# Performance work log

Measured on AMD Instinct MI355X. Metric: run time of the kernel, lower is better.

Reference implementation:

```python
import jax, jax.numpy as jnp
import numpy as np

B, I, H = 512, 256, 512
UNFOLDS = 6


def setup_inputs() -> dict:
    key = jax.random.key(0)
    ks = jax.random.split(key, 13)
    u = lambda k, shape, lo, hi: jax.random.uniform(k, shape, jnp.float32, lo, hi)
    sensory_erev = (2.0 * jax.random.randint(ks[3], (I, H), 0, 2) - 1.0).astype(jnp.float32)
    erev = (2.0 * jax.random.randint(ks[7], (H, H), 0, 2) - 1.0).astype(jnp.float32)
    return {
        "inputs": jax.random.normal(ks[0], (B, I), jnp.float32),
        "state": jax.random.normal(ks[1], (B, H), jnp.float32),
        "sensory_mu": u(ks[2], (I, H), 0.3, 0.8),
        "sensory_sigma": u(ks[4], (I, H), 3.0, 8.0),
        "sensory_W": u(ks[5], (I, H), 0.01, 1.0),
        "sensory_erev": sensory_erev,
        "mu": u(ks[6], (H, H), 0.3, 0.8),
        "sigma": u(ks[8], (H, H), 3.0, 8.0),
        "W": u(ks[9], (H, H), 0.01, 1.0),
        "erev": erev,
        "vleak": u(ks[10], (H,), -0.2, 0.2),
        "gleak": jnp.ones((H,), jnp.float32),
        "cm": jnp.full((H,), 0.5, jnp.float32),
    }


def reference(inputs, state, sensory_mu, sensory_sigma, sensory_W, sensory_erev,
              mu, sigma, W, erev, vleak, gleak, cm):
    # Sensory synapse currents (computed once): (B, I, H) broadcast
    sensory_act = jax.nn.sigmoid((inputs[:, :, None] - sensory_mu[None]) * sensory_sigma[None])
    sensory_w_act = sensory_W[None] * sensory_act                      # (B, I, H)
    w_num_sensory = jnp.sum(sensory_w_act * sensory_erev[None], axis=1)  # (B, H)
    w_den_sensory = jnp.sum(sensory_w_act, axis=1)                        # (B, H)

    def step(v_pre, _):
        # recurrent synapse gating: (B, H_pre, H_post)
        act = jax.nn.sigmoid((v_pre[:, :, None] - mu[None]) * sigma[None])
        w_act = W[None] * act
        w_num = jnp.sum(w_act * erev[None], axis=1) + w_num_sensory
        w_den = jnp.sum(w_act, axis=1) + w_den_sensory
        numerator = cm * v_pre + gleak * vleak + w_num
        denominator = cm + gleak + w_den
        return numerator / (denominator + 1e-8), None

    v_pre, _ = jax.lax.scan(step, state, None, length=UNFOLDS)
    return v_pre
```

## Files before the change

kernel.cpp:

```cpp
#include <hip/hip_runtime.h>

#define LTC_B 512
#define LTC_H 512
#define LTC_I 256

static constexpr float kL2E = 1.4426950408889634f;

struct alignas(8)  H4   { _Float16 a, c, wz, wd; };
struct alignas(16) H4x2 { H4 e[2]; };

typedef unsigned int u32;
#define AS_G __attribute__((address_space(1)))
#define AS_L __attribute__((address_space(3)))

__device__ __forceinline__ void ldg_lds16(const void* g, void* l) {
    __builtin_amdgcn_global_load_lds((const AS_G u32*)g, (AS_L u32*)l, 16, 0, 0);
}

__global__ void ltc_prep(const float* __restrict__ mu, const float* __restrict__ sigma,
                         const float* __restrict__ W, const float* __restrict__ erev,
                         H4x2* __restrict__ slab, int K) {
    int idx = blockIdx.x * 256 + threadIdx.x;
    if (idx >= K * LTC_H) return;
    int j = idx >> 9, h = idx & 511;
    float sg = sigma[idx], m = mu[idx], w = W[idx], ev = erev[idx];
    H4 o;
    o.a  = (_Float16)(-sg * kL2E);
    o.c  = (_Float16)(m * sg * kL2E);
    o.wz = (_Float16)(w * ev);
    o.wd = (_Float16)(w);
    slab[((h >> 6) * (K >> 1) + (j >> 1)) * 64 + (h & 63)].e[j & 1] = o;
}

template<int K, bool RECUR>
__global__ __launch_bounds__(256, 4)
void ltc_pass(const float* __restrict__ vsrc,
              const H4x2* __restrict__ slab,
              const float* __restrict__ snum, const float* __restrict__ sden,
              const float* __restrict__ vleak, const float* __restrict__ gleak,
              const float* __restrict__ cm,
              float* __restrict__ onum, float* __restrict__ oden,
              float* __restrict__ vout)
{
    __shared__ H4x2 wbuf[2][16 * 64];
    const int tid  = threadIdx.x;
    const int lane = tid & 63;
    const int wave = tid >> 6;
    const int ht   = blockIdx.x;
    const int b    = blockIdx.y * 4 + wave;

    constexpr int NG = K / 64;
    float vr[NG];
    #pragma unroll
    for (int g = 0; g < NG; ++g) vr[g] = vsrc[b * K + g * 64 + lane];

    const char* slabt = (const char*)slab + (size_t)ht * (K * 512);
    constexpr int NC = K / 32;
    float n = 0.f, d = 0.f;

    {
        char* dst = (char*)&wbuf[0][0];
        #pragma unroll
        for (int r = 0; r < 4; ++r) {
            const int row = wave * 4 + r;
            ldg_lds16(slabt + row * 1024 + lane * 16, dst + row * 1024);
        }
    }

    #pragma unroll
    for (int c = 0; c < NC; ++c) {
        __syncthreads();
        if (c + 1 < NC) {
            const char* src = slabt + (c + 1) * 16384;
            char* dst = (char*)&wbuf[(c + 1) & 1][0];
            #pragma unroll
            for (int r = 0; r < 4; ++r) {
                const int row = wave * 4 + r;
                ldg_lds16(src + row * 1024 + lane * 16, dst + row * 1024);
            }
        }
        const H4x2* wb = &wbuf[c & 1][0];
        constexpr int dummy = 0; (void)dummy;
        const int g = c >> 1;
        const int joff = (c & 1) * 32;
        #pragma unroll
        for (int jj = 0; jj < 16; ++jj) {
            H4x2 pr = wb[jj * 64 + lane];
            float vj0 = __int_as_float(__builtin_amdgcn_readlane(__float_as_int(vr[g]), joff + jj * 2));
            float vj1 = __int_as_float(__builtin_amdgcn_readlane(__float_as_int(vr[g]), joff + jj * 2 + 1));
            float t0 = fmaf((float)pr.e[0].a, vj0, (float)pr.e[0].c);
            float t1 = fmaf((float)pr.e[1].a, vj1, (float)pr.e[1].c);
            float e0 = __builtin_amdgcn_exp2f(t0);
            float e1 = __builtin_amdgcn_exp2f(t1);
            float s0 = __builtin_amdgcn_rcpf(1.0f + e0);
            float s1 = __builtin_amdgcn_rcpf(1.0f + e1);
            n = fmaf((float)pr.e[0].wz, s0, n);
            d = fmaf((float)pr.e[0].wd, s0, d);
            n = fmaf((float)pr.e[1].wz, s1, n);
            d = fmaf((float)pr.e[1].wd, s1, d);
        }
    }

    const int h  = ht * 64 + lane;
    const int bh = b * LTC_H + h;
    if constexpr (RECUR) {
        const float gl = gleak[h], vl = vleak[h], c0 = cm[h];
        const float vp = vsrc[bh];
        float num = fmaf(c0, vp, gl * vl) + n + snum[bh];
        float den = c0 + gl + d + sden[bh];
        vout[bh] = num * __builtin_amdgcn_rcpf(den + 1e-8f);
    } else {
        onum[bh] = n;
        oden[bh] = d;
    }
}

extern "C" void kernel_launch(void* const* d_in, const int* in_sizes, int n_in,
                              void* d_out, int out_size, void* d_ws, size_t ws_size,
                              hipStream_t stream) {
    const float* inputs = (const float*)d_in[0];
    const float* state  = (const float*)d_in[1];
    const float* smu    = (const float*)d_in[2];
    const float* ssig   = (const float*)d_in[3];
    const float* sW     = (const float*)d_in[4];
    const float* serev  = (const float*)d_in[5];
    const float* mu     = (const float*)d_in[6];
    const float* sig    = (const float*)d_in[7];
    const float* W      = (const float*)d_in[8];
    const float* erev   = (const float*)d_in[9];
    const float* vleak  = (const float*)d_in[10];
    const float* gleak  = (const float*)d_in[11];
    const float* cm     = (const float*)d_in[12];

    float* out  = (float*)d_out;
    char*  ws   = (char*)d_ws;
    float* snum = (float*)(ws);
    float* sden = (float*)(ws + 1 * 1048576);
    float* vA   = (float*)(ws + 2 * 1048576);
    H4x2*  rslab = (H4x2*)(ws + 3 * 1048576);
    H4x2*  sslab = (H4x2*)(ws + 5 * 1048576);

    ltc_prep<<<(LTC_H * LTC_H + 255) / 256, 256, 0, stream>>>(mu, sig, W, erev, rslab, LTC_H);
    ltc_prep<<<(LTC_I * LTC_H + 255) / 256, 256, 0, stream>>>(smu, ssig, sW, serev, sslab, LTC_I);

    dim3 grid(LTC_H / 64, LTC_B / 4);
    dim3 blk(256);

    ltc_pass<LTC_I, false><<<grid, blk, 0, stream>>>(
        inputs, sslab, nullptr, nullptr, nullptr, nullptr, nullptr,
        snum, sden, nullptr);

    const float* vin = state;
    float* targets[6] = {vA, out, vA, out, vA, out};
    for (int s = 0; s < 6; ++s) {
        ltc_pass<LTC_H, true><<<grid, blk, 0, stream>>>(
            vin, rslab, snum, sden, vleak, gleak, cm,
            nullptr, nullptr, targets[s]);
        vin = targets[s];
    }
}
```

Before: 336.1 us.

## Repack slab as paired halves, rotate chunk order, share one reciprocal per pair

Repacks the fp16 parameter slab so each 16-byte element holds the a/c/wz/wd values for two j rows, and the prep kernel writes it coalesced with one thread per pair. The pass kernel starts its chunk loop at a rotation that depends on the block index, to spread concurrent blocks across different slab regions. It reads the pre-activations as wave-uniform scalar loads from memory instead of readlane from registers, preloads all 16 pairs from LDS before computing, and replaces two reciprocals with one reciprocal of the product plus two multiplies. The aim is fewer transcendental ops and less L2 hotspotting, at the cost of more registers and a slightly different rounding.

```diff
diff --git a/kernel.cpp b/kernel.cpp
--- a/kernel.cpp
+++ b/kernel.cpp
@@ -6,8 +6,7 @@
 
 static constexpr float kL2E = 1.4426950408889634f;
 
-struct alignas(8)  H4   { _Float16 a, c, wz, wd; };
-struct alignas(16) H4x2 { H4 e[2]; };
+struct alignas(16) HPair { _Float16 a0, a1, c0, c1, wz0, wz1, wd0, wd1; };
 
 typedef unsigned int u32;
 #define AS_G __attribute__((address_space(1)))
@@ -17,87 +16,99 @@
     __builtin_amdgcn_global_load_lds((const AS_G u32*)g, (AS_L u32*)l, 16, 0, 0);
 }
 
+template<int K>
 __global__ void ltc_prep(const float* __restrict__ mu, const float* __restrict__ sigma,
                          const float* __restrict__ W, const float* __restrict__ erev,
-                         H4x2* __restrict__ slab, int K) {
-    int idx = blockIdx.x * 256 + threadIdx.x;
-    if (idx >= K * LTC_H) return;
-    int j = idx >> 9, h = idx & 511;
-    float sg = sigma[idx], m = mu[idx], w = W[idx], ev = erev[idx];
-    H4 o;
-    o.a  = (_Float16)(-sg * kL2E);
-    o.c  = (_Float16)(m * sg * kL2E);
-    o.wz = (_Float16)(w * ev);
-    o.wd = (_Float16)(w);
-    slab[((h >> 6) * (K >> 1) + (j >> 1)) * 64 + (h & 63)].e[j & 1] = o;
+                         HPair* __restrict__ slab) {
+    const int t = blockIdx.x * 256 + threadIdx.x;
+    if (t >= K * 256) return;
+    const int hh   = t & 63;
+    const int rest = t >> 6;
+    const int jp   = rest & (K / 2 - 1);
+    const int ht   = rest / (K / 2);
+    const int h    = ht * 64 + hh;
+    const int g0   = (2 * jp) * LTC_H + h;
+    const int g1   = g0 + LTC_H;
+    HPair o;
+    o.a0 = (_Float16)(-sigma[g0] * kL2E);
+    o.a1 = (_Float16)(-sigma[g1] * kL2E);
+    o.c0 = (_Float16)(mu[g0] * sigma[g0] * kL2E);
+    o.c1 = (_Float16)(mu[g1] * sigma[g1] * kL2E);
+    o.wz0 = (_Float16)(W[g0] * erev[g0]);
+    o.wz1 = (_Float16)(W[g1] * erev[g1]);
+    o.wd0 = (_Float16)(W[g0]);
+    o.wd1 = (_Float16)(W[g1]);
+    slab[t] = o;
 }
 
 template<int K, bool RECUR>
 __global__ __launch_bounds__(256, 4)
 void ltc_pass(const float* __restrict__ vsrc,
-              const H4x2* __restrict__ slab,
+              const HPair* __restrict__ slab,
               const float* __restrict__ snum, const float* __restrict__ sden,
               const float* __restrict__ vleak, const float* __restrict__ gleak,
               const float* __restrict__ cm,
               float* __restrict__ onum, float* __restrict__ oden,
               float* __restrict__ vout)
 {
-    __shared__ H4x2 wbuf[2][16 * 64];
+    __shared__ HPair wbuf[2][16 * 64];
     const int tid  = threadIdx.x;
     const int lane = tid & 63;
-    const int wave = tid >> 6;
+    const int wu   = __builtin_amdgcn_readfirstlane(tid >> 6);
     const int ht   = blockIdx.x;
-    const int b    = blockIdx.y * 4 + wave;
+    const int b    = blockIdx.y * 4 + wu;
+    const float* __restrict__ vrow = vsrc + (size_t)b * K;
 
-    constexpr int NG = K / 64;
-    float vr[NG];
-    #pragma unroll
-    for (int g = 0; g < NG; ++g) vr[g] = vsrc[b * K + g * 64 + lane];
-
+    constexpr int NC = K / 32;
+    const int rot = (int)((blockIdx.x + 7u * blockIdx.y) & (NC - 1));
     const char* slabt = (const char*)slab + (size_t)ht * (K * 512);
-    constexpr int NC = K / 32;
-    float n = 0.f, d = 0.f;
 
     {
-        char* dst = (char*)&wbuf[0][0];
+        const char* src = slabt + rot * 16384 + wu * 4096;
+        char* dst = (char*)&wbuf[0][0] + wu * 4096;
         #pragma unroll
-        for (int r = 0; r < 4; ++r) {
-            const int row = wave * 4 + r;
-            ldg_lds16(slabt + row * 1024 + lane * 16, dst + row * 1024);
-        }
+        for (int rr = 0; rr < 4; ++rr)
+            ldg_lds16(src + rr * 1024 + lane * 16, dst + rr * 1024);
     }
 
+    float na = 0.f, da = 0.f;
+
     #pragma unroll
-    for (int c = 0; c < NC; ++c) {
+    for (int i = 0; i < NC; ++i) {
+        const int c = (rot + i) & (NC - 1);
         __syncthreads();
-        if (c + 1 < NC) {
-            const char* src = slabt + (c + 1) * 16384;
-            char* dst = (char*)&wbuf[(c + 1) & 1][0];
+        if (i + 1 < NC) {
+            const int cn = (rot + i + 1) & (NC - 1);
+            const char* src = slabt + cn * 16384 + wu * 4096;
+            char* dst = (char*)&wbuf[(i + 1) & 1][0] + wu * 4096;
             #pragma unroll
-            for (int r = 0; r < 4; ++r) {
-                const int row = wave * 4 + r;
-                ldg_lds16(src + row * 1024 + lane * 16, dst + row * 1024);
-            }
+            for (int rr = 0; rr < 4; ++rr)
+                ldg_lds16(src + rr * 1024 + lane * 16, dst + rr * 1024);
         }
-        const H4x2* wb = &wbuf[c & 1][0];
-        constexpr int dummy = 0; (void)dummy;
-        const int g = c >> 1;
-        const int joff = (c & 1) * 32;
+        const HPair* wb = &wbuf[i & 1][0];
+        const float* __restrict__ vch = vrow + c * 32;
+
+        HPair pr[16];
+        #pragma unroll
+        for (int jj = 0; jj < 16; ++jj) pr[jj] = wb[jj * 64 + lane];
+
         #pragma unroll
         for (int jj = 0; jj < 16; ++jj) {
-            H4x2 pr = wb[jj * 64 + lane];
-            float vj0 = __int_as_float(__builtin_amdgcn_readlane(__float_as_int(vr[g]), joff + jj * 2));
-            float vj1 = __int_as_float(__builtin_amdgcn_readlane(__float_as_int(vr[g]), joff + jj * 2 + 1));
-            float t0 = fmaf((float)pr.e[0].a, vj0, (float)pr.e[0].c);
-            float t1 = fmaf((float)pr.e[1].a, vj1, (float)pr.e[1].c);
-            float e0 = __builtin_amdgcn_exp2f(t0);
-            float e1 = __builtin_amdgcn_exp2f(t1);
-            float s0 = __builtin_amdgcn_rcpf(1.0f + e0);
-            float s1 = __builtin_amdgcn_rcpf(1.0f + e1);
-            n = fmaf((float)pr.e[0].wz, s0, n);
-            d = fmaf((float)pr.e[0].wd, s0, d);
-            n = fmaf((float)pr.e[1].wz, s1, n);
-            d = fmaf((float)pr.e[1].wd, s1, d);
+            const float vj0 = vch[2 * jj];
+            const float vj1 = vch[2 * jj + 1];
+            const float t0 = fmaf((float)pr[jj].a0, vj0, (float)pr[jj].c0);
+            const float t1 = fmaf((float)pr[jj].a1, vj1, (float)pr[jj].c1);
+            const float e0 = __builtin_amdgcn_exp2f(t0);
+            const float e1 = __builtin_amdgcn_exp2f(t1);
+            const float d0 = 1.0f + e0;
+            const float d1 = 1.0f + e1;
+            const float rr = __builtin_amdgcn_rcpf(d0 * d1);
+            const float s0 = rr * d1;
+            const float s1 = rr * d0;
+            na = fmaf((float)pr[jj].wz0, s0, na);
+            da = fmaf((float)pr[jj].wd0, s0, da);
+            na = fmaf((float)pr[jj].wz1, s1, na);
+            da = fmaf((float)pr[jj].wd1, s1, da);
         }
     }
 
@@ -106,12 +117,12 @@
     if constexpr (RECUR) {
         const float gl = gleak[h], vl = vleak[h], c0 = cm[h];
         const float vp = vsrc[bh];
-        float num = fmaf(c0, vp, gl * vl) + n + snum[bh];
-        float den = c0 + gl + d + sden[bh];
+        const float num = fmaf(c0, vp, gl * vl) + na + snum[bh];
+        const float den = c0 + gl + da + sden[bh];
         vout[bh] = num * __builtin_amdgcn_rcpf(den + 1e-8f);
     } else {
-        onum[bh] = n;
-        oden[bh] = d;
+        onum[bh] = na;
+        oden[bh] = da;
     }
 }
 
@@ -137,11 +148,11 @@
     float* snum = (float*)(ws);
     float* sden = (float*)(ws + 1 * 1048576);
     float* vA   = (float*)(ws + 2 * 1048576);
-    H4x2*  rslab = (H4x2*)(ws + 3 * 1048576);
-    H4x2*  sslab = (H4x2*)(ws + 5 * 1048576);
+    HPair* rslab = (HPair*)(ws + 3 * 1048576);
+    HPair* sslab = (HPair*)(ws + 5 * 1048576);
 
-    ltc_prep<<<(LTC_H * LTC_H + 255) / 256, 256, 0, stream>>>(mu, sig, W, erev, rslab, LTC_H);
-    ltc_prep<<<(LTC_I * LTC_H + 255) / 256, 256, 0, stream>>>(smu, ssig, sW, serev, sslab, LTC_I);
+    ltc_prep<LTC_H><<<LTC_H * 256 / 256, 256, 0, stream>>>(mu, sig, W, erev, rslab);
+    ltc_prep<LTC_I><<<LTC_I * 256 / 256, 256, 0, stream>>>(smu, ssig, sW, serev, sslab);
 
     dim3 grid(LTC_H / 64, LTC_B / 4);
     dim3 blk(256);
```

Measured after the change: 334.4 us. Within noise of the previous version (-0.5%).
